# Kernel tuning notes

Measured on AMD Instinct MI355X. Metric: run time of the kernel, lower is better.

## Reference

```python
import jax, jax.numpy as jnp
import numpy as np

RESO = 32          # grid_resolution
HID = 32           # hidden_dim
CDIM = 32          # c_dim
NBLK = 5           # n_blocks
PAD = 0.1          # padding
L = 10             # positional encoding frequencies -> dim 60


def setup_inputs() -> dict:
    key = jax.random.key(0)
    ks = jax.random.split(key, 12)
    B, T = 2, 200000
    p = jax.random.uniform(ks[0], (B, T, 3), jnp.float32, -0.5, 0.5)
    s = 0.05
    return {
        "p": p,
        "fc_pos_w": jax.random.normal(ks[1], (60, 2 * HID), jnp.float32) * s,
        "fc_pos_b": jax.random.normal(ks[2], (2 * HID,), jnp.float32) * s,
        "blk_fc0_w": jax.random.normal(ks[3], (NBLK, 2 * HID, HID), jnp.float32) * s,
        "blk_fc0_b": jax.random.normal(ks[4], (NBLK, HID), jnp.float32) * s,
        "blk_fc1_w": jax.random.normal(ks[5], (NBLK, HID, HID), jnp.float32) * s,
        "blk_fc1_b": jax.random.normal(ks[6], (NBLK, HID), jnp.float32) * s,
        "blk_sc_w": jax.random.normal(ks[7], (NBLK, 2 * HID, HID), jnp.float32) * s,  # shortcut, no bias
        "fc_c_w": jax.random.normal(ks[8], (HID, CDIM), jnp.float32) * s,
        "fc_c_b": jax.random.normal(ks[9], (CDIM,), jnp.float32) * s,
    }


def _pos_encode(p):
    # p in [-0.5,0.5] -> [-2,0] after 2p-1 (matches torch impl: p = 2*p - 1)
    q = 2.0 * p - 1.0
    freqs = (jnp.pi * (2.0 ** jnp.arange(L, dtype=jnp.float32)))  # [L]
    a = q[..., None, :] * freqs[:, None]                          # [B,T,L,3]
    pe = jnp.stack([jnp.sin(a), jnp.cos(a)], axis=-2)             # [B,T,L,2,3]
    return pe.reshape(*p.shape[:-1], 2 * L * 3)                   # [B,T,60]


def _normalize_3d(p):
    p_nor = p / (1.0 + PAD + 1e-3) + 0.5
    return jnp.clip(p_nor, 0.0, 1.0 - 1e-3)


def _coord2index(p_nor):
    x = jnp.floor(p_nor * RESO).astype(jnp.int32)                  # [B,T,3]
    return x[..., 0] + RESO * (x[..., 1] + RESO * x[..., 2])       # [B,T]


def _resblock(x, w0, b0, w1, b1, ws):
    h = jax.nn.relu(jax.nn.relu(x) @ w0 + b0)
    return x @ ws + (jax.nn.relu(h) @ w1 + b1)


def reference(p, fc_pos_w, fc_pos_b, blk_fc0_w, blk_fc0_b, blk_fc1_w, blk_fc1_b,
              blk_sc_w, fc_c_w, fc_c_b):
    B, T, _ = p.shape
    G = RESO ** 3
    p_nor = _normalize_3d(p)
    idx = _coord2index(p_nor)                                      # [B,T]
    gidx = (idx + jnp.arange(B, dtype=jnp.int32)[:, None] * G).reshape(-1)  # [B*T]

    net = _pos_encode(p) @ fc_pos_w + fc_pos_b                     # [B,T,64]
    net = _resblock(net, blk_fc0_w[0], blk_fc0_b[0], blk_fc1_w[0], blk_fc1_b[0], blk_sc_w[0])
    for i in range(1, NBLK):
        # pool_local: scatter_max per grid cell, gather back to points
        flat = net.reshape(B * T, HID)
        cell = jax.ops.segment_max(flat, gidx, num_segments=B * G)  # [B*G,HID]
        pooled = cell[gidx].reshape(B, T, HID)
        net = jnp.concatenate([net, pooled], axis=-1)               # [B,T,64]
        net = _resblock(net, blk_fc0_w[i], blk_fc0_b[i], blk_fc1_w[i], blk_fc1_b[i], blk_sc_w[i])

    c = net @ fc_c_w + fc_c_b                                       # [B,T,CDIM]

    # generate_grid_features: scatter_mean into grid (empty cells = 0)
    cf = c.reshape(B * T, CDIM)
    sums = jax.ops.segment_sum(cf, gidx, num_segments=B * G)        # [B*G,CDIM]
    cnt = jax.ops.segment_sum(jnp.ones((B * T, 1), c.dtype), gidx, num_segments=B * G)
    mean = sums / jnp.maximum(cnt, 1.0)
    fea_grid = mean.reshape(B, G, CDIM).transpose(0, 2, 1).reshape(B, CDIM, RESO, RESO, RESO)
    return fea_grid
```

## Files before the change

### kernel.cpp

```cpp
#include <hip/hip_runtime.h>
#include <math.h>

#define TPTS 200000
#define BB 2
#define NPTS (BB*TPTS)
#define GRID3 32768
#define BG 65536
#define SROWS 176

typedef __attribute__((ext_vector_type(8))) __bf16 bf16x8;
typedef __attribute__((ext_vector_type(4))) float f32x4;
typedef unsigned short ushort_t;

#define MFMA16(a,b,c) __builtin_amdgcn_mfma_f32_16x16x32_bf16(a,b,c,0,0,0)

__device__ __forceinline__ void split8(const float* v, bf16x8& hi, bf16x8& lo)
{
#pragma unroll
  for (int j = 0; j < 8; j++) {
    float f = v[j];
    __bf16 h = (__bf16)f;
    hi[j] = h;
    lo[j] = (__bf16)(f - (float)h);
  }
}

__device__ __forceinline__ int cellof(float p0, float p1, float p2, int t)
{
  const float DEN = (float)(1.0 + 0.1 + 1e-3);
  const float HI  = (float)(1.0 - 1e-3);
  float n0 = fminf(fmaxf(p0/DEN + 0.5f, 0.f), HI);
  float n1 = fminf(fmaxf(p1/DEN + 0.5f, 0.f), HI);
  float n2 = fminf(fmaxf(p2/DEN + 0.5f, 0.f), HI);
  int c0 = (int)floorf(n0*32.f), c1 = (int)floorf(n1*32.f), c2 = (int)floorf(n2*32.f);
  return c0 + 32*(c1 + 32*c2) + (t >= TPTS ? GRID3 : 0);
}

__global__ __launch_bounds__(256) void k_hist(
    const float* __restrict__ p, int* __restrict__ gbuf, int* __restrict__ hist)
{
  int t = blockIdx.x*256 + threadIdx.x;
  if (t >= NPTS) return;
  int g = cellof(p[3*t], p[3*t+1], p[3*t+2], t);
  gbuf[t] = g;
  atomicAdd(hist + g, 1);
}

__global__ __launch_bounds__(256) void k_scanA(
    const int* __restrict__ hist, int* __restrict__ texcl, int* __restrict__ bsum)
{
  __shared__ int sm[256];
  int tid = threadIdx.x;
  int t = blockIdx.x*256 + tid;
  int v = hist[t];
  sm[tid] = v; __syncthreads();
  for (int off = 1; off < 256; off <<= 1) {
    int x = sm[tid];
    int u = (tid >= off) ? sm[tid-off] : 0;
    __syncthreads();
    sm[tid] = x + u;
    __syncthreads();
  }
  texcl[t] = sm[tid] - v;
  if (tid == 255) bsum[blockIdx.x] = sm[255];
}

__global__ __launch_bounds__(256) void k_scanB(
    const int* __restrict__ bsum, int* __restrict__ boff)
{
  __shared__ int sm[256];
  int tid = threadIdx.x;
  int v = bsum[tid];
  sm[tid] = v; __syncthreads();
  for (int off = 1; off < 256; off <<= 1) {
    int x = sm[tid];
    int u = (tid >= off) ? sm[tid-off] : 0;
    __syncthreads();
    sm[tid] = x + u;
    __syncthreads();
  }
  boff[tid] = sm[tid] - v;
}

__global__ __launch_bounds__(256) void k_scanC(
    const int* __restrict__ texcl, const int* __restrict__ boff,
    int* __restrict__ start, int* __restrict__ cursor)
{
  int t = blockIdx.x*256 + threadIdx.x;
  int v = boff[blockIdx.x] + texcl[t];
  start[t] = v; cursor[t] = v;
  if (t == 0) start[BG] = NPTS;
}

__global__ __launch_bounds__(256) void k_scatter(
    const float* __restrict__ p, const int* __restrict__ gbuf,
    int* __restrict__ cursor, float* __restrict__ p_sorted, int* __restrict__ gsort)
{
  int t = blockIdx.x*256 + threadIdx.x;
  if (t >= NPTS) return;
  int g = gbuf[t];
  int slot = atomicAdd(cursor + g, 1);
  gsort[slot] = g;
  p_sorted[3*slot]   = p[3*t];
  p_sorted[3*slot+1] = p[3*t+1];
  p_sorted[3*slot+2] = p[3*t+2];
}

__global__ void k_pack(
    const float* __restrict__ f0w, const float* __restrict__ scw,
    const float* __restrict__ f1w, const float* __restrict__ wc,
    const float* __restrict__ Wp,
    ushort_t* __restrict__ wpack)
{
  int f = blockIdx.x, l = threadIdx.x;
  if (f >= 104) {
    int idx = f - 104;
    int c = idx >> 3, t = (idx >> 1) & 3, e = idx & 1;
#pragma unroll
    for (int j = 0; j < 8; j++) {
      int k = c*32 + (l>>4)*8 + j, n = t*16 + (l&15);
      float v = (k < 60) ? Wp[k*64 + n] : 0.f;
      __bf16 h = (__bf16)v;
      __bf16 out = (e == 0) ? h : (__bf16)(v - (float)h);
      union { __bf16 b; ushort_t u; } cv; cv.b = out;
      wpack[((size_t)f*64 + l)*8 + j] = cv.u;
    }
    return;
  }
  const float* W; int c, t, e;
  if (f < 100) {
    int s = f / 20, r = f % 20;
    if (r < 8)       { W = f0w + s*2048; c = r>>2;        t = (r>>1)&1; e = r&1; }
    else if (r < 16) { int q = r-8;  W = scw + s*2048; c = q>>2; t = (q>>1)&1; e = q&1; }
    else             { int q = r-16; W = f1w + s*1024; c = 0;    t = q>>1;     e = q&1; }
  } else { int q = f-100; W = wc; c = 0; t = q>>1; e = q&1; }
#pragma unroll
  for (int j = 0; j < 8; j++) {
    int k = c*32 + (l>>4)*8 + j, n = t*16 + (l&15);
    float v = W[k*32 + n];
    __bf16 h = (__bf16)v;
    __bf16 out = (e == 0) ? h : (__bf16)(v - (float)h);
    union { __bf16 b; ushort_t u; } cv; cv.b = out;
    wpack[((size_t)f*64 + l)*8 + j] = cv.u;
  }
}

__global__ __launch_bounds__(256) void k_fused0(
    const float* __restrict__ ps,
    const ushort_t* __restrict__ wpPE, const float* __restrict__ bp,
    const ushort_t* __restrict__ wp,
    const float* __restrict__ b0, const float* __restrict__ b1,
    float* __restrict__ net)
{
  __shared__ float xlds[4][16*68];
  __shared__ float hbuf[4][16*36];
  int wave = threadIdx.x >> 6, lane = threadIdx.x & 63;
  int m = lane & 15, q = lane >> 4;
  int pbase = (blockIdx.x*4 + wave)*16;
  int pt = pbase + m;

  float p0 = ps[3*pt], p1 = ps[3*pt+1], p2 = ps[3*pt+2];
  float u0 = 2.f*p0 - 1.f, u1 = 2.f*p1 - 1.f, u2 = 2.f*p2 - 1.f;
  const float PIF = 3.14159265358979323846f;

  float pe[2][8];
#pragma unroll
  for (int c2 = 0; c2 < 2; c2++) {
#pragma unroll
    for (int jj = 0; jj < 8; jj++) {
      int e = c2*32 + q*8 + jj;
      int l = (e * 43691) >> 18;
      int r = e - l*6;
      bool issin = (r < 3);
      int d = issin ? r : (r - 3);
      float ud = (d == 0) ? u0 : ((d == 1) ? u1 : u2);
      float xval = ldexpf(ud, l);
      float red = xval - 2.f*rintf(0.5f*xval);
      float ang = PIF*red + (issin ? 0.f : 1.5707963267948966f);
      float v = __sinf(ang);
      pe[c2][jj] = (e < 60) ? v : 0.f;
    }
  }
  bf16x8 peh[2], pel[2];
  split8(pe[0], peh[0], pel[0]);
  split8(pe[1], peh[1], pel[1]);

  f32x4 xacc[4];
#pragma unroll
  for (int t = 0; t < 4; t++) {
    float bb = bp[t*16 + m];
    xacc[t] = (f32x4){bb,bb,bb,bb};
  }
#pragma unroll
  for (int c2 = 0; c2 < 2; c2++)
#pragma unroll
    for (int t = 0; t < 4; t++) {
      bf16x8 bh = *(const bf16x8*)(wpPE + ((size_t)((c2*4+t)*2    )*64 + lane)*8);
      bf16x8 bl = *(const bf16x8*)(wpPE + ((size_t)((c2*4+t)*2 + 1)*64 + lane)*8);
      xacc[t] = MFMA16(peh[c2], bh, xacc[t]);
      xacc[t] = MFMA16(pel[c2], bh, xacc[t]);
      xacc[t] = MFMA16(peh[c2], bl, xacc[t]);
    }

  float* xl = xlds[wave];
#pragma unroll
  for (int t = 0; t < 4; t++)
#pragma unroll
    for (int r = 0; r < 4; r++)
      xl[(q*4+r)*68 + t*16 + m] = xacc[t][r];
  __syncthreads();

  float xv[2][8];
#pragma unroll
  for (int c2 = 0; c2 < 2; c2++)
#pragma unroll
    for (int jj = 0; jj < 8; jj++)
      xv[c2][jj] = xl[m*68 + c2*32 + q*8 + jj];

  bf16x8 w0f[2][2][2], wsf[2][2][2], w1f[2][2];
#pragma unroll
  for (int c = 0; c < 2; c++)
#pragma unroll
    for (int t = 0; t < 2; t++)
#pragma unroll
      for (int e = 0; e < 2; e++) {
        w0f[c][t][e] = *(const bf16x8*)(wp + ((size_t)(((c*2+t)*2+e)    )*64 + lane)*8);
        wsf[c][t][e] = *(const bf16x8*)(wp + ((size_t)(((c*2+t)*2+e) + 8)*64 + lane)*8);
      }
#pragma unroll
  for (int t = 0; t < 2; t++)
#pragma unroll
    for (int e = 0; e < 2; e++)
      w1f[t][e] = *(const bf16x8*)(wp + ((size_t)(16 + t*2 + e)*64 + lane)*8);

  bf16x8 axh[2], axl[2], arh[2], arl[2];
#pragma unroll
  for (int c = 0; c < 2; c++) {
    float r[8];
#pragma unroll
    for (int j = 0; j < 8; j++) r[j] = fmaxf(xv[c][j], 0.f);
    split8(xv[c], axh[c], axl[c]);
    split8(r,     arh[c], arl[c]);
  }

  f32x4 hacc[2], yacc[2];
#pragma unroll
  for (int t = 0; t < 2; t++) {
    float bb0 = b0[m + 16*t], bb1 = b1[m + 16*t];
    hacc[t] = (f32x4){bb0,bb0,bb0,bb0};
    yacc[t] = (f32x4){bb1,bb1,bb1,bb1};
  }

#pragma unroll
  for (int c = 0; c < 2; c++)
#pragma unroll
    for (int t = 0; t < 2; t++) {
      hacc[t] = MFMA16(arh[c], w0f[c][t][0], hacc[t]);
      hacc[t] = MFMA16(arl[c], w0f[c][t][0], hacc[t]);
      hacc[t] = MFMA16(arh[c], w0f[c][t][1], hacc[t]);
      yacc[t] = MFMA16(axh[c], wsf[c][t][0], yacc[t]);
      yacc[t] = MFMA16(axl[c], wsf[c][t][0], yacc[t]);
      yacc[t] = MFMA16(axh[c], wsf[c][t][1], yacc[t]);
    }

  float* hb = hbuf[wave];
#pragma unroll
  for (int t = 0; t < 2; t++)
#pragma unroll
    for (int r = 0; r < 4; r++)
      hb[(q*4+r)*36 + m + 16*t] = fmaxf(hacc[t][r], 0.f);
  __syncthreads();
  float hv[8];
#pragma unroll
  for (int j = 0; j < 8; j++) hv[j] = hb[m*36 + q*8 + j];
  bf16x8 hh, hl; split8(hv, hh, hl);
#pragma unroll
  for (int t = 0; t < 2; t++) {
    yacc[t] = MFMA16(hh, w1f[t][0], yacc[t]);
    yacc[t] = MFMA16(hl, w1f[t][0], yacc[t]);
    yacc[t] = MFMA16(hh, w1f[t][1], yacc[t]);
  }

#pragma unroll
  for (int t = 0; t < 2; t++)
#pragma unroll
    for (int r = 0; r < 4; r++)
      net[(size_t)(pbase + q*4 + r)*32 + m + 16*t] = yacc[t][r];
}

__global__ __launch_bounds__(256) void k_stage_f(
    const float* __restrict__ netin, float* __restrict__ netout,
    const int* __restrict__ gsort, const int* __restrict__ start,
    const ushort_t* __restrict__ wp,
    const float* __restrict__ b0, const float* __restrict__ b1)
{
  __shared__ float sbuf[SROWS*36];
  int tid = threadIdx.x;
  int P0 = blockIdx.x*64;
  int s = start[gsort[P0]];
  int e = start[gsort[P0+63] + 1];
  int n = e - s; if (n > SROWS) n = SROWS;

  for (int idx = tid; idx < n*8; idx += 256) {
    int r = idx >> 3, c = idx & 7;
    *(f32x4*)(sbuf + r*36 + c*4) =
      *(const f32x4*)(netin + ((size_t)(s + r))*32 + c*4);
  }
  __syncthreads();

  int wave = tid >> 6, lane = tid & 63;
  int m = lane & 15, q = lane >> 4;
  int pbase = P0 + wave*16;
  int pt = pbase + m;
  int g = gsort[pt];
  int cs = start[g] - s, ce = start[g+1] - s;

  float xv[2][8];
  {
    const float* xr = sbuf + (pt - s)*36 + q*8;
    *(f32x4*)&xv[0][0] = *(const f32x4*)xr;
    *(f32x4*)&xv[0][4] = *(const f32x4*)(xr + 4);
  }
  {
    f32x4 ma = (f32x4){-INFINITY,-INFINITY,-INFINITY,-INFINITY};
    f32x4 mb = ma;
    for (int k = cs; k < ce; k++) {
      const float* rr = sbuf + k*36 + q*8;
      f32x4 va = *(const f32x4*)rr;
      f32x4 vb = *(const f32x4*)(rr + 4);
      ma.x = fmaxf(ma.x, va.x); ma.y = fmaxf(ma.y, va.y);
      ma.z = fmaxf(ma.z, va.z); ma.w = fmaxf(ma.w, va.w);
      mb.x = fmaxf(mb.x, vb.x); mb.y = fmaxf(mb.y, vb.y);
      mb.z = fmaxf(mb.z, vb.z); mb.w = fmaxf(mb.w, vb.w);
    }
    *(f32x4*)&xv[1][0] = ma;
    *(f32x4*)&xv[1][4] = mb;
  }

  bf16x8 w0f[2][2][2], wsf[2][2][2], w1f[2][2];
#pragma unroll
  for (int c = 0; c < 2; c++)
#pragma unroll
    for (int t = 0; t < 2; t++)
#pragma unroll
      for (int e2 = 0; e2 < 2; e2++) {
        w0f[c][t][e2] = *(const bf16x8*)(wp + ((size_t)(((c*2+t)*2+e2)    )*64 + lane)*8);
        wsf[c][t][e2] = *(const bf16x8*)(wp + ((size_t)(((c*2+t)*2+e2) + 8)*64 + lane)*8);
      }
#pragma unroll
  for (int t = 0; t < 2; t++)
#pragma unroll
    for (int e2 = 0; e2 < 2; e2++)
      w1f[t][e2] = *(const bf16x8*)(wp + ((size_t)(16 + t*2 + e2)*64 + lane)*8);

  bf16x8 axh[2], axl[2], arh[2], arl[2];
#pragma unroll
  for (int c = 0; c < 2; c++) {
    float r[8];
#pragma unroll
    for (int j = 0; j < 8; j++) r[j] = fmaxf(xv[c][j], 0.f);
    split8(xv[c], axh[c], axl[c]);
    split8(r,     arh[c], arl[c]);
  }

  f32x4 hacc[2], yacc[2];
#pragma unroll
  for (int t = 0; t < 2; t++) {
    float bb0 = b0[m + 16*t], bb1 = b1[m + 16*t];
    hacc[t] = (f32x4){bb0,bb0,bb0,bb0};
    yacc[t] = (f32x4){bb1,bb1,bb1,bb1};
  }

#pragma unroll
  for (int c = 0; c < 2; c++)
#pragma unroll
    for (int t = 0; t < 2; t++) {
      hacc[t] = MFMA16(arh[c], w0f[c][t][0], hacc[t]);
      hacc[t] = MFMA16(arl[c], w0f[c][t][0], hacc[t]);
      hacc[t] = MFMA16(arh[c], w0f[c][t][1], hacc[t]);
      yacc[t] = MFMA16(axh[c], wsf[c][t][0], yacc[t]);
      yacc[t] = MFMA16(axl[c], wsf[c][t][0], yacc[t]);
      yacc[t] = MFMA16(axh[c], wsf[c][t][1], yacc[t]);
    }

  __syncthreads();
  float* hb = sbuf + wave*576;
#pragma unroll
  for (int t = 0; t < 2; t++)
#pragma unroll
    for (int r = 0; r < 4; r++)
      hb[(q*4+r)*36 + m + 16*t] = fmaxf(hacc[t][r], 0.f);
  __syncthreads();
  float hv[8];
#pragma unroll
  for (int j = 0; j < 8; j++) hv[j] = hb[m*36 + q*8 + j];
  bf16x8 hh, hl; split8(hv, hh, hl);
#pragma unroll
  for (int t = 0; t < 2; t++) {
    yacc[t] = MFMA16(hh, w1f[t][0], yacc[t]);
    yacc[t] = MFMA16(hl, w1f[t][0], yacc[t]);
    yacc[t] = MFMA16(hh, w1f[t][1], yacc[t]);
  }

#pragma unroll
  for (int t = 0; t < 2; t++)
#pragma unroll
    for (int r = 0; r < 4; r++)
      netout[(size_t)(pbase + q*4 + r)*32 + m + 16*t] = yacc[t][r];
}

__global__ __launch_bounds__(256) void k_final_f(
    const float* __restrict__ netin, float* __restrict__ netout,
    const int* __restrict__ gsort, const int* __restrict__ start,
    const ushort_t* __restrict__ wp, const ushort_t* __restrict__ wpc,
    const float* __restrict__ b0, const float* __restrict__ b1,
    const float* __restrict__ bc)
{
  __shared__ float sbuf[SROWS*36];
  int tid = threadIdx.x;
  int P0 = blockIdx.x*64;
  int s = start[gsort[P0]];
  int e = start[gsort[P0+63] + 1];
  int n = e - s; if (n > SROWS) n = SROWS;

  for (int idx = tid; idx < n*8; idx += 256) {
    int r = idx >> 3, c = idx & 7;
    *(f32x4*)(sbuf + r*36 + c*4) =
      *(const f32x4*)(netin + ((size_t)(s + r))*32 + c*4);
  }
  __syncthreads();

  int wave = tid >> 6, lane = tid & 63;
  int m = lane & 15, q = lane >> 4;
  int pbase = P0 + wave*16;
  int pt = pbase + m;
  int g = gsort[pt];
  int cs = start[g] - s, ce = start[g+1] - s;

  float xv[2][8];
  {
    const float* xr = sbuf + (pt - s)*36 + q*8;
    *(f32x4*)&xv[0][0] = *(const f32x4*)xr;
    *(f32x4*)&xv[0][4] = *(const f32x4*)(xr + 4);
  }
  {
    f32x4 ma = (f32x4){-INFINITY,-INFINITY,-INFINITY,-INFINITY};
    f32x4 mb = ma;
    for (int k = cs; k < ce; k++) {
      const float* rr = sbuf + k*36 + q*8;
      f32x4 va = *(const f32x4*)rr;
      f32x4 vb = *(const f32x4*)(rr + 4);
      ma.x = fmaxf(ma.x, va.x); ma.y = fmaxf(ma.y, va.y);
      ma.z = fmaxf(ma.z, va.z); ma.w = fmaxf(ma.w, va.w);
      mb.x = fmaxf(mb.x, vb.x); mb.y = fmaxf(mb.y, vb.y);
      mb.z = fmaxf(mb.z, vb.z); mb.w = fmaxf(mb.w, vb.w);
    }
    *(f32x4*)&xv[1][0] = ma;
    *(f32x4*)&xv[1][4] = mb;
  }

  bf16x8 w0f[2][2][2], wsf[2][2][2], w1f[2][2], wcf[2][2];
#pragma unroll
  for (int c = 0; c < 2; c++)
#pragma unroll
    for (int t = 0; t < 2; t++)
#pragma unroll
      for (int e2 = 0; e2 < 2; e2++) {
        w0f[c][t][e2] = *(const bf16x8*)(wp + ((size_t)(((c*2+t)*2+e2)    )*64 + lane)*8);
        wsf[c][t][e2] = *(const bf16x8*)(wp + ((size_t)(((c*2+t)*2+e2) + 8)*64 + lane)*8);
      }
#pragma unroll
  for (int t = 0; t < 2; t++)
#pragma unroll
    for (int e2 = 0; e2 < 2; e2++) {
      w1f[t][e2] = *(const bf16x8*)(wp  + ((size_t)(16 + t*2 + e2)*64 + lane)*8);
      wcf[t][e2] = *(const bf16x8*)(wpc + ((size_t)(     t*2 + e2)*64 + lane)*8);
    }

  bf16x8 axh[2], axl[2], arh[2], arl[2];
#pragma unroll
  for (int c = 0; c < 2; c++) {
    float r[8];
#pragma unroll
    for (int j = 0; j < 8; j++) r[j] = fmaxf(xv[c][j], 0.f);
    split8(xv[c], axh[c], axl[c]);
    split8(r,     arh[c], arl[c]);
  }

  f32x4 hacc[2], yacc[2];
#pragma unroll
  for (int t = 0; t < 2; t++) {
    float bb0 = b0[m + 16*t], bb1 = b1[m + 16*t];
    hacc[t] = (f32x4){bb0,bb0,bb0,bb0};
    yacc[t] = (f32x4){bb1,bb1,bb1,bb1};
  }

#pragma unroll
  for (int c = 0; c < 2; c++)
#pragma unroll
    for (int t = 0; t < 2; t++) {
      hacc[t] = MFMA16(arh[c], w0f[c][t][0], hacc[t]);
      hacc[t] = MFMA16(arl[c], w0f[c][t][0], hacc[t]);
      hacc[t] = MFMA16(arh[c], w0f[c][t][1], hacc[t]);
      yacc[t] = MFMA16(axh[c], wsf[c][t][0], yacc[t]);
      yacc[t] = MFMA16(axl[c], wsf[c][t][0], yacc[t]);
      yacc[t] = MFMA16(axh[c], wsf[c][t][1], yacc[t]);
    }

  __syncthreads();
  float* hb = sbuf + wave*576;
  float* yb = sbuf + 4*576 + wave*576;
#pragma unroll
  for (int t = 0; t < 2; t++)
#pragma unroll
    for (int r = 0; r < 4; r++)
      hb[(q*4+r)*36 + m + 16*t] = fmaxf(hacc[t][r], 0.f);
  __syncthreads();
  float hv[8];
#pragma unroll
  for (int j = 0; j < 8; j++) hv[j] = hb[m*36 + q*8 + j];
  bf16x8 hh, hl; split8(hv, hh, hl);
#pragma unroll
  for (int t = 0; t < 2; t++) {
    yacc[t] = MFMA16(hh, w1f[t][0], yacc[t]);
    yacc[t] = MFMA16(hl, w1f[t][0], yacc[t]);
    yacc[t] = MFMA16(hh, w1f[t][1], yacc[t]);
  }

#pragma unroll
  for (int t = 0; t < 2; t++)
#pragma unroll
    for (int r = 0; r < 4; r++)
      yb[(q*4+r)*36 + m + 16*t] = yacc[t][r];
  __syncthreads();
  float yv[8];
#pragma unroll
  for (int j = 0; j < 8; j++) yv[j] = yb[m*36 + q*8 + j];
  bf16x8 yh, yl; split8(yv, yh, yl);

  f32x4 cacc[2];
#pragma unroll
  for (int t = 0; t < 2; t++) {
    float bb = bc[m + 16*t];
    cacc[t] = (f32x4){bb,bb,bb,bb};
    cacc[t] = MFMA16(yh, wcf[t][0], cacc[t]);
    cacc[t] = MFMA16(yl, wcf[t][0], cacc[t]);
    cacc[t] = MFMA16(yh, wcf[t][1], cacc[t]);
  }

#pragma unroll
  for (int t = 0; t < 2; t++)
#pragma unroll
    for (int r = 0; r < 4; r++)
      netout[(size_t)(pbase + q*4 + r)*32 + m + 16*t] = cacc[t][r];
}

__global__ __launch_bounds__(256) void k_mean(
    const float* __restrict__ net, const int* __restrict__ start,
    float* __restrict__ outp)
{
  int tid = blockIdx.x*256 + threadIdx.x;
  int c = tid >> 3, sub = tid & 7;
  int s = start[c], e = start[c+1];
  f32x4 sum = (f32x4){0.f,0.f,0.f,0.f};
  for (int k = s; k < e; k++) {
    f32x4 v = *(const f32x4*)(net + (size_t)k*32 + sub*4);
    sum.x += v.x; sum.y += v.y; sum.z += v.z; sum.w += v.w;
  }
  float inv = (e > s) ? 1.f/(float)(e - s) : 0.f;
  int b = c >> 15, cell = c & 32767;
  size_t ob = ((size_t)b << 20) + cell;
#pragma unroll
  for (int jj = 0; jj < 4; jj++) {
    int ch = sub*4 + jj;
    float v = ((const float*)&sum)[jj] * inv;
    outp[ob + ((size_t)ch << 15)] = v;
  }
}

extern "C" void kernel_launch(void* const* d_in, const int* in_sizes, int n_in,
                              void* d_out, int out_size, void* d_ws, size_t ws_size,
                              hipStream_t stream)
{
  const float* p   = (const float*)d_in[0];
  const float* Wp  = (const float*)d_in[1];
  const float* bp  = (const float*)d_in[2];
  const float* f0w = (const float*)d_in[3];
  const float* f0b = (const float*)d_in[4];
  const float* f1w = (const float*)d_in[5];
  const float* f1b = (const float*)d_in[6];
  const float* scw = (const float*)d_in[7];
  const float* wc  = (const float*)d_in[8];
  const float* bc  = (const float*)d_in[9];
  float* outp = (float*)d_out;

  char* wsb = (char*)d_ws;
  float*    netA     = (float*)wsb;
  float*    netB     = netA + (size_t)NPTS*32;
  int*      gbuf     = (int*)(netB + (size_t)NPTS*32);
  int*      gsort    = gbuf + NPTS;
  int*      hist     = gsort + NPTS;
  int*      start    = hist + BG;
  int*      cursor   = start + BG + 1;
  int*      texcl    = cursor + BG;
  int*      bsum     = texcl + BG;
  int*      boff     = bsum + 256;
  ushort_t* wpack    = (ushort_t*)(boff + 256);
  float*    p_sorted = (float*)(wpack + (size_t)120*512);

  dim3 blk(256);
  dim3 gpts((NPTS + 255)/256);
  dim3 gmfma(NPTS/64);
  dim3 gcell((BG*8)/256);
  dim3 gscan(BG/256);

  hipMemsetAsync(hist, 0, (size_t)BG*4, stream);
  hipLaunchKernelGGL(k_hist, gpts, blk, 0, stream, p, gbuf, hist);
  hipLaunchKernelGGL(k_scanA, gscan, blk, 0, stream, hist, texcl, bsum);
  hipLaunchKernelGGL(k_scanB, dim3(1), blk, 0, stream, bsum, boff);
  hipLaunchKernelGGL(k_scanC, gscan, blk, 0, stream, texcl, boff, start, cursor);
  hipLaunchKernelGGL(k_scatter, gpts, blk, 0, stream, p, gbuf, cursor, p_sorted, gsort);
  hipLaunchKernelGGL(k_pack, dim3(120), dim3(64), 0, stream, f0w, scw, f1w, wc, Wp, wpack);
  hipLaunchKernelGGL(k_fused0, gmfma, blk, 0, stream,
                     p_sorted, wpack + (size_t)104*512, bp,
                     wpack + (size_t)0*20*512, f0b + 0*32, f1b + 0*32, netA);
  hipLaunchKernelGGL(k_stage_f, gmfma, blk, 0, stream, netA, netB, gsort, start,
                     wpack + (size_t)1*20*512, f0b + 1*32, f1b + 1*32);
  hipLaunchKernelGGL(k_stage_f, gmfma, blk, 0, stream, netB, netA, gsort, start,
                     wpack + (size_t)2*20*512, f0b + 2*32, f1b + 2*32);
  hipLaunchKernelGGL(k_stage_f, gmfma, blk, 0, stream, netA, netB, gsort, start,
                     wpack + (size_t)3*20*512, f0b + 3*32, f1b + 3*32);
  hipLaunchKernelGGL(k_final_f, gmfma, blk, 0, stream, netB, netA, gsort, start,
                     wpack + (size_t)4*20*512, wpack + (size_t)100*512,
                     f0b + 4*32, f1b + 4*32, bc);
  hipLaunchKernelGGL(k_mean, gcell, blk, 0, stream, netA, start, outp);
}
```

Baseline: 331.4 us.

## Fuse scatter-mean into final stage by recomputing whole cells per block

The final resblock kernel now computes the block-4 MLP and fc_c for every row in the block's cell-aligned shared window, not only its own 64 points. Each block then writes the per-cell mean for any cell whose first point lies in its range directly to the output grid. This removes the separate k_mean kernel and the global write and reread of the point features. In exchange, rows near block edges are computed twice, the output needs a memset for empty cells, and correctness depends on every cell fitting within the SROWS window.

```diff
diff --git a/kernel.cpp b/kernel.cpp
--- a/kernel.cpp
+++ b/kernel.cpp
@@ -410,18 +410,21 @@
 }
 
 __global__ __launch_bounds__(256) void k_final_f(
-    const float* __restrict__ netin, float* __restrict__ netout,
+    const float* __restrict__ netin,
     const int* __restrict__ gsort, const int* __restrict__ start,
     const ushort_t* __restrict__ wp, const ushort_t* __restrict__ wpc,
     const float* __restrict__ b0, const float* __restrict__ b1,
-    const float* __restrict__ bc)
+    const float* __restrict__ bc,
+    float* __restrict__ outp)
 {
   __shared__ float sbuf[SROWS*36];
+  __shared__ float hbuf[4*576];
   int tid = threadIdx.x;
   int P0 = blockIdx.x*64;
   int s = start[gsort[P0]];
   int e = start[gsort[P0+63] + 1];
   int n = e - s; if (n > SROWS) n = SROWS;
+  int T = (n + 15) >> 4;
 
   for (int idx = tid; idx < n*8; idx += 256) {
     int r = idx >> 3, c = idx & 7;
@@ -432,32 +435,7 @@
 
   int wave = tid >> 6, lane = tid & 63;
   int m = lane & 15, q = lane >> 4;
-  int pbase = P0 + wave*16;
-  int pt = pbase + m;
-  int g = gsort[pt];
-  int cs = start[g] - s, ce = start[g+1] - s;
-
-  float xv[2][8];
-  {
-    const float* xr = sbuf + (pt - s)*36 + q*8;
-    *(f32x4*)&xv[0][0] = *(const f32x4*)xr;
-    *(f32x4*)&xv[0][4] = *(const f32x4*)(xr + 4);
-  }
-  {
-    f32x4 ma = (f32x4){-INFINITY,-INFINITY,-INFINITY,-INFINITY};
-    f32x4 mb = ma;
-    for (int k = cs; k < ce; k++) {
-      const float* rr = sbuf + k*36 + q*8;
-      f32x4 va = *(const f32x4*)rr;
-      f32x4 vb = *(const f32x4*)(rr + 4);
-      ma.x = fmaxf(ma.x, va.x); ma.y = fmaxf(ma.y, va.y);
-      ma.z = fmaxf(ma.z, va.z); ma.w = fmaxf(ma.w, va.w);
-      mb.x = fmaxf(mb.x, vb.x); mb.y = fmaxf(mb.y, vb.y);
-      mb.z = fmaxf(mb.z, vb.z); mb.w = fmaxf(mb.w, vb.w);
-    }
-    *(f32x4*)&xv[1][0] = ma;
-    *(f32x4*)&xv[1][4] = mb;
-  }
+  float* hb = hbuf + wave*576;
 
   bf16x8 w0f[2][2][2], wsf[2][2][2], w1f[2][2], wcf[2][2];
 #pragma unroll
@@ -477,104 +455,146 @@
       wcf[t][e2] = *(const bf16x8*)(wpc + ((size_t)(     t*2 + e2)*64 + lane)*8);
     }
 
-  bf16x8 axh[2], axl[2], arh[2], arl[2];
-#pragma unroll
-  for (int c = 0; c < 2; c++) {
-    float r[8];
-#pragma unroll
-    for (int j = 0; j < 8; j++) r[j] = fmaxf(xv[c][j], 0.f);
-    split8(xv[c], axh[c], axl[c]);
-    split8(r,     arh[c], arl[c]);
-  }
-
-  f32x4 hacc[2], yacc[2];
-#pragma unroll
-  for (int t = 0; t < 2; t++) {
-    float bb0 = b0[m + 16*t], bb1 = b1[m + 16*t];
-    hacc[t] = (f32x4){bb0,bb0,bb0,bb0};
-    yacc[t] = (f32x4){bb1,bb1,bb1,bb1};
-  }
-
-#pragma unroll
-  for (int c = 0; c < 2; c++)
-#pragma unroll
-    for (int t = 0; t < 2; t++) {
-      hacc[t] = MFMA16(arh[c], w0f[c][t][0], hacc[t]);
-      hacc[t] = MFMA16(arl[c], w0f[c][t][0], hacc[t]);
-      hacc[t] = MFMA16(arh[c], w0f[c][t][1], hacc[t]);
-      yacc[t] = MFMA16(axh[c], wsf[c][t][0], yacc[t]);
-      yacc[t] = MFMA16(axl[c], wsf[c][t][0], yacc[t]);
-      yacc[t] = MFMA16(axh[c], wsf[c][t][1], yacc[t]);
-    }
-
-  __syncthreads();
-  float* hb = sbuf + wave*576;
-  float* yb = sbuf + 4*576 + wave*576;
-#pragma unroll
-  for (int t = 0; t < 2; t++)
-#pragma unroll
-    for (int r = 0; r < 4; r++)
-      hb[(q*4+r)*36 + m + 16*t] = fmaxf(hacc[t][r], 0.f);
-  __syncthreads();
-  float hv[8];
-#pragma unroll
-  for (int j = 0; j < 8; j++) hv[j] = hb[m*36 + q*8 + j];
-  bf16x8 hh, hl; split8(hv, hh, hl);
-#pragma unroll
-  for (int t = 0; t < 2; t++) {
-    yacc[t] = MFMA16(hh, w1f[t][0], yacc[t]);
-    yacc[t] = MFMA16(hl, w1f[t][0], yacc[t]);
-    yacc[t] = MFMA16(hh, w1f[t][1], yacc[t]);
-  }
-
-#pragma unroll
-  for (int t = 0; t < 2; t++)
-#pragma unroll
-    for (int r = 0; r < 4; r++)
-      yb[(q*4+r)*36 + m + 16*t] = yacc[t][r];
-  __syncthreads();
-  float yv[8];
-#pragma unroll
-  for (int j = 0; j < 8; j++) yv[j] = yb[m*36 + q*8 + j];
-  bf16x8 yh, yl; split8(yv, yh, yl);
-
-  f32x4 cacc[2];
-#pragma unroll
-  for (int t = 0; t < 2; t++) {
-    float bb = bc[m + 16*t];
-    cacc[t] = (f32x4){bb,bb,bb,bb};
-    cacc[t] = MFMA16(yh, wcf[t][0], cacc[t]);
-    cacc[t] = MFMA16(yl, wcf[t][0], cacc[t]);
-    cacc[t] = MFMA16(yh, wcf[t][1], cacc[t]);
-  }
-
-#pragma unroll
-  for (int t = 0; t < 2; t++)
-#pragma unroll
-    for (int r = 0; r < 4; r++)
-      netout[(size_t)(pbase + q*4 + r)*32 + m + 16*t] = cacc[t][r];
-}
-
-__global__ __launch_bounds__(256) void k_mean(
-    const float* __restrict__ net, const int* __restrict__ start,
-    float* __restrict__ outp)
-{
-  int tid = blockIdx.x*256 + threadIdx.x;
-  int c = tid >> 3, sub = tid & 7;
-  int s = start[c], e = start[c+1];
-  f32x4 sum = (f32x4){0.f,0.f,0.f,0.f};
-  for (int k = s; k < e; k++) {
-    f32x4 v = *(const f32x4*)(net + (size_t)k*32 + sub*4);
-    sum.x += v.x; sum.y += v.y; sum.z += v.z; sum.w += v.w;
-  }
-  float inv = (e > s) ? 1.f/(float)(e - s) : 0.f;
-  int b = c >> 15, cell = c & 32767;
-  size_t ob = ((size_t)b << 20) + cell;
-#pragma unroll
-  for (int jj = 0; jj < 4; jj++) {
-    int ch = sub*4 + jj;
-    float v = ((const float*)&sum)[jj] * inv;
-    outp[ob + ((size_t)ch << 15)] = v;
+#define FTILE(TT, Y0out, Y1out) do {                                          \
+    int rbase = (TT)*16;                                                      \
+    int rr0 = rbase + m;                                                      \
+    int rsX = (rr0 < n) ? rr0 : (n - 1);                                      \
+    float xv[2][8];                                                           \
+    { const float* xr = sbuf + rsX*36 + q*8;                                  \
+      *(f32x4*)&xv[0][0] = *(const f32x4*)xr;                                 \
+      *(f32x4*)&xv[0][4] = *(const f32x4*)(xr + 4); }                         \
+    { int gX = gsort[s + rsX];                                                \
+      int csX = start[gX] - s, ceX = start[gX+1] - s; if (ceX > n) ceX = n;   \
+      f32x4 ma = (f32x4){-INFINITY,-INFINITY,-INFINITY,-INFINITY};            \
+      f32x4 mb = ma;                                                          \
+      for (int k = csX; k < ceX; k++) {                                       \
+        const float* rr2 = sbuf + k*36 + q*8;                                 \
+        f32x4 va = *(const f32x4*)rr2;                                        \
+        f32x4 vb = *(const f32x4*)(rr2 + 4);                                  \
+        ma.x = fmaxf(ma.x, va.x); ma.y = fmaxf(ma.y, va.y);                   \
+        ma.z = fmaxf(ma.z, va.z); ma.w = fmaxf(ma.w, va.w);                   \
+        mb.x = fmaxf(mb.x, vb.x); mb.y = fmaxf(mb.y, vb.y);                   \
+        mb.z = fmaxf(mb.z, vb.z); mb.w = fmaxf(mb.w, vb.w);                   \
+      }                                                                       \
+      *(f32x4*)&xv[1][0] = ma;                                                \
+      *(f32x4*)&xv[1][4] = mb; }                                              \
+    bf16x8 axh[2], axl[2], arh[2], arl[2];                                    \
+    _Pragma("unroll")                                                         \
+    for (int c = 0; c < 2; c++) {                                             \
+      float rv[8];                                                            \
+      _Pragma("unroll")                                                       \
+      for (int j = 0; j < 8; j++) rv[j] = fmaxf(xv[c][j], 0.f);               \
+      split8(xv[c], axh[c], axl[c]);                                          \
+      split8(rv,    arh[c], arl[c]);                                          \
+    }                                                                         \
+    f32x4 hacc[2], yacc[2];                                                   \
+    _Pragma("unroll")                                                         \
+    for (int t2 = 0; t2 < 2; t2++) {                                          \
+      float bb0 = b0[m + 16*t2], bb1 = b1[m + 16*t2];                         \
+      hacc[t2] = (f32x4){bb0,bb0,bb0,bb0};                                    \
+      yacc[t2] = (f32x4){bb1,bb1,bb1,bb1};                                    \
+    }                                                                         \
+    _Pragma("unroll")                                                         \
+    for (int c = 0; c < 2; c++)                                               \
+      _Pragma("unroll")                                                       \
+      for (int t2 = 0; t2 < 2; t2++) {                                        \
+        hacc[t2] = MFMA16(arh[c], w0f[c][t2][0], hacc[t2]);                   \
+        hacc[t2] = MFMA16(arl[c], w0f[c][t2][0], hacc[t2]);                   \
+        hacc[t2] = MFMA16(arh[c], w0f[c][t2][1], hacc[t2]);                   \
+        yacc[t2] = MFMA16(axh[c], wsf[c][t2][0], yacc[t2]);                   \
+        yacc[t2] = MFMA16(axl[c], wsf[c][t2][0], yacc[t2]);                   \
+        yacc[t2] = MFMA16(axh[c], wsf[c][t2][1], yacc[t2]);                   \
+      }                                                                       \
+    _Pragma("unroll")                                                         \
+    for (int t2 = 0; t2 < 2; t2++)                                            \
+      _Pragma("unroll")                                                       \
+      for (int r2 = 0; r2 < 4; r2++)                                          \
+        hb[(q*4+r2)*36 + m + 16*t2] = fmaxf(hacc[t2][r2], 0.f);               \
+    __threadfence_block();                                                    \
+    { float hv[8];                                                            \
+      _Pragma("unroll")                                                       \
+      for (int j = 0; j < 8; j++) hv[j] = hb[m*36 + q*8 + j];                 \
+      bf16x8 hh, hl; split8(hv, hh, hl);                                      \
+      _Pragma("unroll")                                                       \
+      for (int t2 = 0; t2 < 2; t2++) {                                        \
+        yacc[t2] = MFMA16(hh, w1f[t2][0], yacc[t2]);                          \
+        yacc[t2] = MFMA16(hl, w1f[t2][0], yacc[t2]);                          \
+        yacc[t2] = MFMA16(hh, w1f[t2][1], yacc[t2]);                          \
+      } }                                                                     \
+    __threadfence_block();                                                    \
+    Y0out = yacc[0]; Y1out = yacc[1];                                         \
+  } while (0)
+
+  f32x4 yA0, yA1, yB0, yB1, yC0, yC1;
+  {
+    int t0 = wave, t1 = wave + 4, t2 = wave + 8;
+    if (t0 < T) FTILE(t0, yA0, yA1);
+    if (t1 < T) FTILE(t1, yB0, yB1);
+    if (t2 < T) FTILE(t2, yC0, yC1);
+  }
+  __syncthreads();
+
+#define CTILE(TT, Y0in, Y1in) do {                                            \
+    int rbase = (TT)*16;                                                      \
+    _Pragma("unroll")                                                         \
+    for (int r2 = 0; r2 < 4; r2++) {                                          \
+      sbuf[(rbase + q*4 + r2)*36 + m]      = Y0in[r2];                        \
+      sbuf[(rbase + q*4 + r2)*36 + m + 16] = Y1in[r2];                        \
+    }                                                                         \
+    __threadfence_block();                                                    \
+    float yv[8];                                                              \
+    { const float* yr = sbuf + (rbase + m)*36 + q*8;                          \
+      *(f32x4*)&yv[0] = *(const f32x4*)yr;                                    \
+      *(f32x4*)&yv[4] = *(const f32x4*)(yr + 4); }                            \
+    bf16x8 yh, yl; split8(yv, yh, yl);                                        \
+    float bb0 = bc[m], bb1 = bc[16+m];                                        \
+    f32x4 c0 = (f32x4){bb0,bb0,bb0,bb0};                                      \
+    f32x4 c1 = (f32x4){bb1,bb1,bb1,bb1};                                      \
+    c0 = MFMA16(yh, wcf[0][0], c0); c0 = MFMA16(yl, wcf[0][0], c0);           \
+    c0 = MFMA16(yh, wcf[0][1], c0);                                           \
+    c1 = MFMA16(yh, wcf[1][0], c1); c1 = MFMA16(yl, wcf[1][0], c1);           \
+    c1 = MFMA16(yh, wcf[1][1], c1);                                           \
+    __threadfence_block();                                                    \
+    _Pragma("unroll")                                                         \
+    for (int r2 = 0; r2 < 4; r2++) {                                          \
+      sbuf[(rbase + q*4 + r2)*36 + m]      = c0[r2];                          \
+      sbuf[(rbase + q*4 + r2)*36 + m + 16] = c1[r2];                          \
+    }                                                                         \
+  } while (0)
+
+  {
+    int t0 = wave, t1 = wave + 4, t2 = wave + 8;
+    if (t0 < T) CTILE(t0, yA0, yA1);
+    if (t1 < T) CTILE(t1, yB0, yB1);
+    if (t2 < T) CTILE(t2, yC0, yC1);
+  }
+  __syncthreads();
+
+  {
+    int o = tid >> 2, qq = tid & 3;
+    int r = (P0 - s) + o;
+    int g2 = gsort[P0 + o];
+    int cs2 = start[g2] - s;
+    if (cs2 == r) {
+      int ce2 = start[g2+1] - s; if (ce2 > n) ce2 = n;
+      f32x4 sa = (f32x4){0.f,0.f,0.f,0.f};
+      f32x4 sb = sa;
+      for (int k = cs2; k < ce2; k++) {
+        const float* rr2 = sbuf + k*36 + qq*8;
+        f32x4 va = *(const f32x4*)rr2;
+        f32x4 vb = *(const f32x4*)(rr2 + 4);
+        sa.x += va.x; sa.y += va.y; sa.z += va.z; sa.w += va.w;
+        sb.x += vb.x; sb.y += vb.y; sb.z += vb.z; sb.w += vb.w;
+      }
+      float inv = 1.f / (float)(ce2 - cs2);
+      int b2 = g2 >> 15, cell = g2 & 32767;
+      size_t ob = ((size_t)b2 << 20) + cell;
+#pragma unroll
+      for (int jj = 0; jj < 4; jj++) {
+        outp[ob + ((size_t)(qq*8 + jj)     << 15)] = sa[jj] * inv;
+        outp[ob + ((size_t)(qq*8 + jj + 4) << 15)] = sb[jj] * inv;
+      }
+    }
   }
 }
 
@@ -611,10 +631,10 @@
   dim3 blk(256);
   dim3 gpts((NPTS + 255)/256);
   dim3 gmfma(NPTS/64);
-  dim3 gcell((BG*8)/256);
   dim3 gscan(BG/256);
 
   hipMemsetAsync(hist, 0, (size_t)BG*4, stream);
+  hipMemsetAsync(outp, 0, (size_t)BG*32*4, stream);
   hipLaunchKernelGGL(k_hist, gpts, blk, 0, stream, p, gbuf, hist);
   hipLaunchKernelGGL(k_scanA, gscan, blk, 0, stream, hist, texcl, bsum);
   hipLaunchKernelGGL(k_scanB, dim3(1), blk, 0, stream, bsum, boff);
@@ -630,8 +650,7 @@
                      wpack + (size_t)2*20*512, f0b + 2*32, f1b + 2*32);
   hipLaunchKernelGGL(k_stage_f, gmfma, blk, 0, stream, netA, netB, gsort, start,
                      wpack + (size_t)3*20*512, f0b + 3*32, f1b + 3*32);
-  hipLaunchKernelGGL(k_final_f, gmfma, blk, 0, stream, netB, netA, gsort, start,
+  hipLaunchKernelGGL(k_final_f, gmfma, blk, 0, stream, netB, gsort, start,
                      wpack + (size_t)4*20*512, wpack + (size_t)100*512,
-                     f0b + 4*32, f1b + 4*32, bc);
-  hipLaunchKernelGGL(k_mean, gcell, blk, 0, stream, netA, start, outp);
-}
+                     f0b + 4*32, f1b + 4*32, bc, outp);
+}
```

Result: slower. 378.6 us (+14.2%).
